# Kernel tuning notes

Hardware: AMD Instinct MI355X
Metric: run time of the kernel (lower is better)

The kernel has to match this reference:

```python
import jax, jax.numpy as jnp
import numpy as np

SEQ, BATCH, HID = 512, 64, 1024

def setup_inputs() -> dict:
    key = jax.random.key(0)
    ks = jax.random.split(key, 10)
    s2 = 1.0 / np.sqrt(2 * HID)
    s1 = 1.0 / np.sqrt(HID)
    return {
        "input": jax.random.normal(ks[0], (SEQ, BATCH, HID), dtype=jnp.float32),
        "prev_state": jax.random.normal(ks[1], (BATCH, HID), dtype=jnp.float32),
        # nn.Linear weights are [out, in], biases [out]
        "W_r": jax.random.uniform(ks[2], (HID, 2 * HID), jnp.float32, -s2, s2),
        "b_r": jax.random.uniform(ks[3], (HID,), jnp.float32, -s2, s2),
        "W_u": jax.random.uniform(ks[4], (HID, 2 * HID), jnp.float32, -s2, s2),
        "b_u": jax.random.uniform(ks[5], (HID,), jnp.float32, -s2, s2),
        "W_o": jax.random.uniform(ks[6], (HID, HID), jnp.float32, -s1, s1),
        "b_o": jax.random.uniform(ks[7], (HID,), jnp.float32, -s1, s1),
        "W_x": jax.random.uniform(ks[8], (HID, HID), jnp.float32, -s1, s1),
        "b_x": jax.random.uniform(ks[9], (HID,), jnp.float32, -s1, s1),
    }


def reference(input, prev_state, W_r, b_r, W_u, b_u, W_o, b_o, W_x, b_x):
    # input: [seq, batch, hid]; prev_state: [batch, hid]
    def step(h, x_t):
        xh = jnp.concatenate([x_t, h], axis=1)          # [batch, 2*hid]
        reset = jax.nn.sigmoid(xh @ W_r.T + b_r)
        update = jax.nn.sigmoid(xh @ W_u.T + b_u)
        cand = jnp.tanh((h @ W_o.T + b_o) * reset + (x_t @ W_x.T + b_x))
        new_h = (1.0 - update) * cand + update * h
        return new_h, new_h

    new_state, hidden_seq = jax.lax.scan(step, prev_state, input)
    return hidden_seq, new_state
```

## Files before the change

### kernel.cpp

```cpp
#include <hip/hip_runtime.h>
#include <hip/hip_bf16.h>

#define SEQ 512
#define BATCH 64
#define HID 1024

typedef __bf16 bf16x8 __attribute__((ext_vector_type(8)));
typedef __bf16 bf16x4 __attribute__((ext_vector_type(4)));
typedef float f32x4 __attribute__((ext_vector_type(4)));

__device__ __forceinline__ float sigm(float x) { return 1.0f / (1.0f + __expf(-x)); }
__device__ __forceinline__ float tanh_(float x) { return 2.0f / (1.0f + __expf(-2.0f * x)) - 1.0f; }

__device__ __forceinline__ void cload_b128(bf16x8* d, const __bf16* p) {
    asm volatile("global_load_dwordx4 %0, %1, off sc0 sc1" : "=v"(*d) : "v"(p));
}
__device__ __forceinline__ void cstore_b16(__bf16* p, __bf16 v) {
    unsigned short uv = __builtin_bit_cast(unsigned short, v);
    asm volatile("global_store_short %0, %1, off sc0 sc1" :: "v"(p), "v"(uv));
}
__device__ __forceinline__ void cstore_b32(unsigned* p, unsigned v) {
    asm volatile("global_store_dword %0, %1, off sc0 sc1" :: "v"(p), "v"(v));
}
__device__ __forceinline__ unsigned cload_b32(const unsigned* p) {
    unsigned r;
    asm volatile("global_load_dword %0, %1, off sc0 sc1\n\ts_waitcnt vmcnt(0)"
                 : "=v"(r) : "v"(p) : "memory");
    __builtin_amdgcn_sched_barrier(0);
    return r;
}
__device__ __forceinline__ void vmcnt0() {
    asm volatile("s_waitcnt vmcnt(0)" ::: "memory");
    __builtin_amdgcn_sched_barrier(0);
}

__global__ __launch_bounds__(256) void cvt_f32_bf16(const float* __restrict__ src,
                                                     __bf16* __restrict__ dst, int n)
{
    int i = (blockIdx.x * 256 + threadIdx.x) * 4;
    if (i < n) {
        f32x4 v = *(const f32x4*)(src + i);
        bf16x4 o;
        #pragma unroll
        for (int j = 0; j < 4; ++j) o[j] = (__bf16)v[j];
        *(bf16x4*)(dst + i) = o;
    }
}


__global__ __launch_bounds__(256) void gru_phaseA2(
    const __bf16* __restrict__ xb,
    const __bf16* __restrict__ Wrb, const __bf16* __restrict__ Wub,
    const __bf16* __restrict__ Wxb,
    const float* __restrict__ br, const float* __restrict__ bu,
    const float* __restrict__ bx, __bf16* __restrict__ G)
{
    __shared__ __bf16 Al[128 * 64];
    __shared__ __bf16 Bl[128 * 64];

    const int NT = 24;
    int mt = blockIdx.x / NT, nt = blockIdx.x % NT;
    int m0 = mt * 128, n0 = nt * 128;

    const __bf16* W; const float* bias; int wstride, nb, gate;
    if (n0 < HID)          { W = Wrb; bias = br; wstride = 2 * HID; nb = n0;           gate = 0; }
    else if (n0 < 2 * HID) { W = Wub; bias = bu; wstride = 2 * HID; nb = n0 - HID;     gate = 1; }
    else                   { W = Wxb; bias = bx; wstride = HID;     nb = n0 - 2 * HID; gate = 2; }

    const int tid = threadIdx.x;
    const int lane = tid & 63, w = tid >> 6;
    const int llo = lane & 15, lhi = lane >> 4;
    const int wm = (w & 1) * 64, wn = (w >> 1) * 64;

    f32x4 acc[4][4] = {};

    for (int k0 = 0; k0 < HID; k0 += 64) {
        __syncthreads();
        #pragma unroll
        for (int s = 0; s < 4; ++s) {
            int idx = s * 256 + tid;
            int r = idx >> 3, c16 = idx & 7;
            int eoff = (c16 * 8) ^ ((r & 7) << 3);
            const __bf16* ga = xb + (size_t)(m0 + r) * HID + k0 + eoff;
            char* la = (char*)Al + (size_t)(s * 256 + w * 64) * 16;
            __builtin_amdgcn_global_load_lds(
                (const __attribute__((address_space(1))) void*)ga,
                (__attribute__((address_space(3))) void*)la, 16, 0, 0);
        }
        #pragma unroll
        for (int s = 0; s < 4; ++s) {
            int idx = s * 256 + tid;
            int r = idx >> 3, c16 = idx & 7;
            int eoff = (c16 * 8) ^ ((r & 7) << 3);
            const __bf16* gb = W + (size_t)(nb + r) * wstride + k0 + eoff;
            char* lb = (char*)Bl + (size_t)(s * 256 + w * 64) * 16;
            __builtin_amdgcn_global_load_lds(
                (const __attribute__((address_space(1))) void*)gb,
                (__attribute__((address_space(3))) void*)lb, 16, 0, 0);
        }
        __syncthreads();

        #pragma unroll
        for (int kk = 0; kk < 2; ++kk) {
            bf16x8 a[4], b[4];
            #pragma unroll
            for (int mi = 0; mi < 4; ++mi) {
                int row = wm + mi * 16 + llo;
                a[mi] = *(const bf16x8*)((const char*)Al + row * 128
                          + ((kk * 64 + lhi * 16) ^ ((row & 7) << 4)));
            }
            #pragma unroll
            for (int ni = 0; ni < 4; ++ni) {
                int row = wn + ni * 16 + llo;
                b[ni] = *(const bf16x8*)((const char*)Bl + row * 128
                          + ((kk * 64 + lhi * 16) ^ ((row & 7) << 4)));
            }
            #pragma unroll
            for (int mi = 0; mi < 4; ++mi)
                #pragma unroll
                for (int ni = 0; ni < 4; ++ni)
                    acc[mi][ni] = __builtin_amdgcn_mfma_f32_16x16x32_bf16(a[mi], b[ni], acc[mi][ni], 0, 0, 0);
        }
    }

    #pragma unroll
    for (int ni = 0; ni < 4; ++ni) {
        int cg0 = nb + wn + ni * 16;
        int jn = cg0 >> 4;
        float bv = bias[cg0 + llo];
        #pragma unroll
        for (int mi = 0; mi < 4; ++mi) {
            #pragma unroll
            for (int i = 0; i < 4; ++i) {
                int m = m0 + wm + mi * 16 + lhi * 4 + i;
                int tt = m >> 6, b = m & 63;
                size_t addr = ((((size_t)tt * 8 + (b >> 3)) * 64 + jn) * 3 + gate) * 128
                            + (b & 7) * 16 + llo;
                G[addr] = (__bf16)(acc[mi][ni][i] + bv);
            }
        }
    }
}

__global__ __launch_bounds__(256) void gru_phaseA_f32(
    const float* __restrict__ xf,
    const __bf16* __restrict__ Wrb, const __bf16* __restrict__ Wub,
    const __bf16* __restrict__ Wxb,
    const float* __restrict__ br, const float* __restrict__ bu,
    const float* __restrict__ bx, __bf16* __restrict__ G)
{
    const int NT = (3 * HID) / 64;
    int mt = blockIdx.x / NT;
    int nt = blockIdx.x % NT;
    int m0 = mt * 128, n0 = nt * 64;

    const __bf16* W; const float* bias; int wstride, nb, gate;
    if (n0 < HID)          { W = Wrb; bias = br; wstride = 2 * HID; nb = n0;           gate = 0; }
    else if (n0 < 2 * HID) { W = Wub; bias = bu; wstride = 2 * HID; nb = n0 - HID;     gate = 1; }
    else                   { W = Wxb; bias = bx; wstride = HID;     nb = n0 - 2 * HID; gate = 2; }

    int lane = threadIdx.x & 63, w = threadIdx.x >> 6;
    int llo = lane & 15, lhi = lane >> 4;
    int wm = (w & 1) * 64, wn = (w >> 1) * 32;

    f32x4 acc[4][2] = {};
    #pragma unroll 2
    for (int k0 = 0; k0 < HID; k0 += 32) {
        int ka = k0 + lhi * 8;
        bf16x8 af[4], bfr[2];
        #pragma unroll
        for (int mi = 0; mi < 4; ++mi) {
            size_t roff = (size_t)(m0 + wm + mi * 16 + llo) * HID + ka;
            f32x4 lo = *(const f32x4*)(xf + roff);
            f32x4 hi = *(const f32x4*)(xf + roff + 4);
            #pragma unroll
            for (int jj = 0; jj < 4; ++jj) { af[mi][jj] = (__bf16)lo[jj]; af[mi][4 + jj] = (__bf16)hi[jj]; }
        }
        #pragma unroll
        for (int ni = 0; ni < 2; ++ni)
            bfr[ni] = *(const bf16x8*)(W + (size_t)(nb + wn + ni * 16 + llo) * wstride + ka);
        #pragma unroll
        for (int mi = 0; mi < 4; ++mi)
            #pragma unroll
            for (int ni = 0; ni < 2; ++ni)
                acc[mi][ni] = __builtin_amdgcn_mfma_f32_16x16x32_bf16(af[mi], bfr[ni], acc[mi][ni], 0, 0, 0);
    }
    #pragma unroll
    for (int ni = 0; ni < 2; ++ni) {
        int cg0 = nb + wn + ni * 16;
        int jn = cg0 >> 4;
        float bv = bias[cg0 + llo];
        #pragma unroll
        for (int mi = 0; mi < 4; ++mi) {
            #pragma unroll
            for (int i = 0; i < 4; ++i) {
                int m = m0 + wm + mi * 16 + lhi * 4 + i;
                int tt = m >> 6, b = m & 63;
                size_t addr = ((((size_t)tt * 8 + (b >> 3)) * 64 + jn) * 3 + gate) * 128
                            + (b & 7) * 16 + llo;
                G[addr] = (__bf16)(acc[mi][ni][i] + bv);
            }
        }
    }
}

__global__ __launch_bounds__(256) void gru_init(const float* __restrict__ prev,
                                                __bf16* __restrict__ hg,
                                                unsigned* __restrict__ flags)
{
    int i = blockIdx.x * 256 + threadIdx.x;
    if (i < 512 * 32) flags[i] = 0u;
    if (i < BATCH * HID) hg[i] = (__bf16)prev[i];
}

__global__ __launch_bounds__(256, 2) void gru_phaseB(
    const __bf16* __restrict__ Wrb, const __bf16* __restrict__ Wub,
    const __bf16* __restrict__ Wob, const float* __restrict__ bo,
    const float* __restrict__ prev, const __bf16* __restrict__ G,
    __bf16* __restrict__ hg, unsigned* __restrict__ flags,
    float* __restrict__ out)
{
    __shared__ float gbuf[2][3][4][128];
    __shared__ __bf16 Gld[2][384];

    const int gwg = blockIdx.x;
    const int j = gwg & 63, rg = gwg >> 6;
    const int tid = threadIdx.x;
    const int lane = tid & 63, ks = tid >> 6;
    const int llo = lane & 15, lhi = lane >> 4;

    bf16x8 wV[3][8];
    {
        const __bf16* w0 = Wrb + (size_t)(16 * j + llo) * (2 * HID) + HID + ks * 256 + lhi * 8;
        const __bf16* w1 = Wub + (size_t)(16 * j + llo) * (2 * HID) + HID + ks * 256 + lhi * 8;
        const __bf16* w2 = Wob + (size_t)(16 * j + llo) * HID + ks * 256 + lhi * 8;
        #pragma unroll
        for (int kk = 0; kk < 8; ++kk) {
            wV[0][kk] = *(const bf16x8*)(w0 + kk * 32);
            wV[1][kk] = *(const bf16x8*)(w1 + kk * 32);
            wV[2][kk] = *(const bf16x8*)(w2 + kk * 32);
        }
    }

    const int erow = 2 * ks + ((lane >> 4) & 1);
    const int ecol = lane & 15;
    float hf = 0.f, bov = 0.f;
    if (lane < 32) {
        hf = prev[(size_t)(8 * rg + erow) * HID + 16 * j + ecol];
        bov = bo[16 * j + ecol];
    }

    if (ks == 0 && lane < 48) {
        const __bf16* gsrc = G + (((size_t)0 * 8 + rg) * 64 + j) * 384 + lane * 8;
        __builtin_amdgcn_global_load_lds(
            (const __attribute__((address_space(1))) void*)gsrc,
            (__attribute__((address_space(3))) void*)((char*)&Gld[0][0] + lane * 16),
            16, 0, 0);
    }

    for (int t = 0; t < SEQ; ++t) {
        const int p = t & 1;
        if (t > 0) {
            const unsigned* fp = flags + (size_t)(rg * 64 + 16 * ks + llo) * 32;
            int guard = 0;
            for (;;) {
                unsigned v = cload_b32(fp);
                if (__all((int)(v >= (unsigned)t))) break;
                if (++guard >= (1 << 20)) break;
            }
        }
        const __bf16* hk = hg + (size_t)p * (BATCH * HID)
                         + (size_t)(8 * rg + (llo & 7)) * HID + ks * 256 + lhi * 8;
        bf16x8 hv[8];
        #pragma unroll
        for (int kk = 0; kk < 8; ++kk) cload_b128(&hv[kk], hk + kk * 32);
        vmcnt0();
        f32x4 aR = {}, aU = {}, aO = {};
        #pragma unroll
        for (int kk = 0; kk < 8; ++kk) {
            aR = __builtin_amdgcn_mfma_f32_16x16x32_bf16(hv[kk], wV[0][kk], aR, 0, 0, 0);
            aU = __builtin_amdgcn_mfma_f32_16x16x32_bf16(hv[kk], wV[1][kk], aU, 0, 0, 0);
            aO = __builtin_amdgcn_mfma_f32_16x16x32_bf16(hv[kk], wV[2][kk], aO, 0, 0, 0);
        }
        if (lhi < 2) {
            #pragma unroll
            for (int i = 0; i < 4; ++i) {
                gbuf[p][0][ks][(lhi * 4 + i) * 16 + llo] = aR[i];
                gbuf[p][1][ks][(lhi * 4 + i) * 16 + llo] = aU[i];
                gbuf[p][2][ks][(lhi * 4 + i) * 16 + llo] = aO[i];
            }
        }
        __syncthreads();

        float hnew = 0.f;
        if (lane < 32) {
            int idx = erow * 16 + ecol;
            float sR = gbuf[p][0][0][idx] + gbuf[p][0][1][idx] + gbuf[p][0][2][idx] + gbuf[p][0][3][idx];
            float sU = gbuf[p][1][0][idx] + gbuf[p][1][1][idx] + gbuf[p][1][2][idx] + gbuf[p][1][3][idx];
            float sO = gbuf[p][2][0][idx] + gbuf[p][2][1][idx] + gbuf[p][2][2][idx] + gbuf[p][2][3][idx];
            float gr = (float)Gld[p][0 * 128 + idx];
            float gu = (float)Gld[p][1 * 128 + idx];
            float gx = (float)Gld[p][2 * 128 + idx];
            float r = sigm(sR + gr);
            float u = sigm(sU + gu);
            float c = tanh_((sO + bov) * r + gx);
            hnew = (1.0f - u) * c + u * hf;
            hf = hnew;
            cstore_b16(hg + (size_t)(p ^ 1) * (BATCH * HID)
                          + (size_t)(8 * rg + erow) * HID + 16 * j + ecol, (__bf16)hnew);
        }
        __syncthreads();
        if (tid == 0)
            cstore_b32(flags + (size_t)(rg * 64 + j) * 32, (unsigned)(t + 1));
        if (ks == 0 && lane < 48 && t + 1 < SEQ) {
            const __bf16* gsrc = G + (((size_t)(t + 1) * 8 + rg) * 64 + j) * 384 + lane * 8;
            __builtin_amdgcn_global_load_lds(
                (const __attribute__((address_space(1))) void*)gsrc,
                (__attribute__((address_space(3))) void*)((char*)&Gld[p ^ 1][0] + lane * 16),
                16, 0, 0);
        }
        if (lane < 32) {
            __builtin_nontemporal_store(hnew,
                out + ((size_t)t * BATCH + 8 * rg + erow) * HID + 16 * j + ecol);
            if (t == SEQ - 1)
                __builtin_nontemporal_store(hnew,
                    out + ((size_t)SEQ * BATCH + 8 * rg + erow) * HID + 16 * j + ecol);
        }
    }
}

extern "C" void kernel_launch(void* const* d_in, const int* in_sizes, int n_in,
                              void* d_out, int out_size, void* d_ws, size_t ws_size,
                              hipStream_t stream) {
    (void)in_sizes; (void)n_in; (void)out_size;
    const float* x    = (const float*)d_in[0];
    const float* prev = (const float*)d_in[1];
    const float* Wr   = (const float*)d_in[2];
    const float* br   = (const float*)d_in[3];
    const float* Wu   = (const float*)d_in[4];
    const float* bu   = (const float*)d_in[5];
    const float* Wo   = (const float*)d_in[6];
    const float* bo   = (const float*)d_in[7];
    const float* Wx   = (const float*)d_in[8];
    const float* bx   = (const float*)d_in[9];
    float* out = (float*)d_out;

    const size_t G_ELEMS  = (size_t)SEQ * BATCH * 3 * HID;
    const size_t WR_ELEMS = (size_t)HID * 2 * HID;
    const size_t WO_ELEMS = (size_t)HID * HID;
    char* ws = (char*)d_ws;
    size_t off = 0;
    __bf16* G   = (__bf16*)(ws + off); off += G_ELEMS * 2;
    __bf16* Wrb = (__bf16*)(ws + off); off += WR_ELEMS * 2;
    __bf16* Wub = (__bf16*)(ws + off); off += WR_ELEMS * 2;
    __bf16* Wob = (__bf16*)(ws + off); off += WO_ELEMS * 2;
    __bf16* Wxb = (__bf16*)(ws + off); off += WO_ELEMS * 2;
    __bf16* hg  = (__bf16*)(ws + off); off += (size_t)2 * BATCH * HID * 2;
    unsigned* flags = (unsigned*)(ws + off); off += 512 * 32 * 4;
    const size_t X_ELEMS = (size_t)SEQ * BATCH * HID;
    bool use_xb = (ws_size >= off + X_ELEMS * 2);
    __bf16* xb = (__bf16*)(ws + off);

    cvt_f32_bf16<<<(int)(WR_ELEMS / 4 / 256), 256, 0, stream>>>(Wr, Wrb, (int)WR_ELEMS);
    cvt_f32_bf16<<<(int)(WR_ELEMS / 4 / 256), 256, 0, stream>>>(Wu, Wub, (int)WR_ELEMS);
    cvt_f32_bf16<<<(int)(WO_ELEMS / 4 / 256), 256, 0, stream>>>(Wo, Wob, (int)WO_ELEMS);
    cvt_f32_bf16<<<(int)(WO_ELEMS / 4 / 256), 256, 0, stream>>>(Wx, Wxb, (int)WO_ELEMS);
    if (use_xb)
        cvt_f32_bf16<<<(int)(X_ELEMS / 4 / 256), 256, 0, stream>>>(x, xb, (int)X_ELEMS);

    gru_init<<<(BATCH * HID) / 256, 256, 0, stream>>>(prev, hg, flags);

    if (use_xb) {
        gru_phaseA2<<<256 * 24, 256, 0, stream>>>(xb, Wrb, Wub, Wxb, br, bu, bx, G);
    } else {
        int gridA = (SEQ * BATCH / 128) * ((3 * HID) / 64);
        gru_phaseA_f32<<<gridA, 256, 0, stream>>>(x, Wrb, Wub, Wxb, br, bu, bx, G);
    }

    gru_phaseB<<<512, 256, 0, stream>>>(Wrb, Wub, Wob, bo, prev, G, hg, flags, out);
}
```

Before: 2.265 ms.

## Use per-wave packed step flags and batch output stores per eight steps

The cross-workgroup step flags are repacked into a dense 2048-entry layout, so a polling wave reads 64 adjacent flags (16 producers × 4 waves) instead of strided, padded slots. Each wave now publishes its own flag right after draining its hidden-state stores, which removes the second __syncthreads from the per-step critical path. Output writes to the hidden sequence are buffered in registers and issued every eight steps. The goal is to shorten the serial per-timestep latency, at the cost of correctness resting more on per-wave memory-ordering and more live registers.

```diff
diff --git a/kernel.cpp b/kernel.cpp
--- a/kernel.cpp
+++ b/kernel.cpp
@@ -209,7 +209,7 @@
                                                 unsigned* __restrict__ flags)
 {
     int i = blockIdx.x * 256 + threadIdx.x;
-    if (i < 512 * 32) flags[i] = 0u;
+    if (i < 2048) flags[i] = 0u;
     if (i < BATCH * HID) hg[i] = (__bf16)prev[i];
 }
 
@@ -250,6 +250,9 @@
         bov = bo[16 * j + ecol];
     }
 
+    unsigned* fstore = flags + (size_t)(rg * 4 + (j >> 4)) * 64 + (j & 15) * 4 + ks;
+    const unsigned* fpoll = flags + (size_t)(rg * 4 + ks) * 64 + (lane & 15) * 4 + (lane >> 4);
+
     if (ks == 0 && lane < 48) {
         const __bf16* gsrc = G + (((size_t)0 * 8 + rg) * 64 + j) * 384 + lane * 8;
         __builtin_amdgcn_global_load_lds(
@@ -258,72 +261,79 @@
             16, 0, 0);
     }
 
-    for (int t = 0; t < SEQ; ++t) {
-        const int p = t & 1;
-        if (t > 0) {
-            const unsigned* fp = flags + (size_t)(rg * 64 + 16 * ks + llo) * 32;
-            int guard = 0;
-            for (;;) {
-                unsigned v = cload_b32(fp);
-                if (__all((int)(v >= (unsigned)t))) break;
-                if (++guard >= (1 << 20)) break;
-            }
-        }
-        const __bf16* hk = hg + (size_t)p * (BATCH * HID)
-                         + (size_t)(8 * rg + (llo & 7)) * HID + ks * 256 + lhi * 8;
-        bf16x8 hv[8];
-        #pragma unroll
-        for (int kk = 0; kk < 8; ++kk) cload_b128(&hv[kk], hk + kk * 32);
-        vmcnt0();
-        f32x4 aR = {}, aU = {}, aO = {};
-        #pragma unroll
-        for (int kk = 0; kk < 8; ++kk) {
-            aR = __builtin_amdgcn_mfma_f32_16x16x32_bf16(hv[kk], wV[0][kk], aR, 0, 0, 0);
-            aU = __builtin_amdgcn_mfma_f32_16x16x32_bf16(hv[kk], wV[1][kk], aU, 0, 0, 0);
-            aO = __builtin_amdgcn_mfma_f32_16x16x32_bf16(hv[kk], wV[2][kk], aO, 0, 0, 0);
-        }
-        if (lhi < 2) {
-            #pragma unroll
-            for (int i = 0; i < 4; ++i) {
-                gbuf[p][0][ks][(lhi * 4 + i) * 16 + llo] = aR[i];
-                gbuf[p][1][ks][(lhi * 4 + i) * 16 + llo] = aU[i];
-                gbuf[p][2][ks][(lhi * 4 + i) * 16 + llo] = aO[i];
-            }
-        }
-        __syncthreads();
-
-        float hnew = 0.f;
+    float ob[8];
+    for (int t0 = 0; t0 < SEQ; t0 += 8) {
+        #pragma unroll
+        for (int s = 0; s < 8; ++s) {
+            const int t = t0 + s;
+            const int p = t & 1;
+            if (t > 0) {
+                int guard = 0;
+                for (;;) {
+                    unsigned v = cload_b32(fpoll);
+                    if (__all((int)(v >= (unsigned)t))) break;
+                    if (++guard >= (1 << 20)) break;
+                }
+            }
+            const __bf16* hk = hg + (size_t)p * (BATCH * HID)
+                             + (size_t)(8 * rg + (llo & 7)) * HID + ks * 256 + lhi * 8;
+            bf16x8 hv[8];
+            #pragma unroll
+            for (int kk = 0; kk < 8; ++kk) cload_b128(&hv[kk], hk + kk * 32);
+            vmcnt0();
+            f32x4 aR = {}, aU = {}, aO = {};
+            #pragma unroll
+            for (int kk = 0; kk < 8; ++kk) {
+                aR = __builtin_amdgcn_mfma_f32_16x16x32_bf16(hv[kk], wV[0][kk], aR, 0, 0, 0);
+                aU = __builtin_amdgcn_mfma_f32_16x16x32_bf16(hv[kk], wV[1][kk], aU, 0, 0, 0);
+                aO = __builtin_amdgcn_mfma_f32_16x16x32_bf16(hv[kk], wV[2][kk], aO, 0, 0, 0);
+            }
+            if (lhi < 2) {
+                #pragma unroll
+                for (int i = 0; i < 4; ++i) {
+                    gbuf[p][0][ks][(lhi * 4 + i) * 16 + llo] = aR[i];
+                    gbuf[p][1][ks][(lhi * 4 + i) * 16 + llo] = aU[i];
+                    gbuf[p][2][ks][(lhi * 4 + i) * 16 + llo] = aO[i];
+                }
+            }
+            __syncthreads();
+
+            float hnew = 0.f;
+            if (lane < 32) {
+                int idx = erow * 16 + ecol;
+                float sR = gbuf[p][0][0][idx] + gbuf[p][0][1][idx] + gbuf[p][0][2][idx] + gbuf[p][0][3][idx];
+                float sU = gbuf[p][1][0][idx] + gbuf[p][1][1][idx] + gbuf[p][1][2][idx] + gbuf[p][1][3][idx];
+                float sO = gbuf[p][2][0][idx] + gbuf[p][2][1][idx] + gbuf[p][2][2][idx] + gbuf[p][2][3][idx];
+                float gr = (float)Gld[p][0 * 128 + idx];
+                float gu = (float)Gld[p][1 * 128 + idx];
+                float gx = (float)Gld[p][2 * 128 + idx];
+                float r = sigm(sR + gr);
+                float u = sigm(sU + gu);
+                float c = tanh_((sO + bov) * r + gx);
+                hnew = (1.0f - u) * c + u * hf;
+                hf = hnew;
+                cstore_b16(hg + (size_t)(p ^ 1) * (BATCH * HID)
+                              + (size_t)(8 * rg + erow) * HID + 16 * j + ecol, (__bf16)hnew);
+            }
+            ob[s] = hnew;
+            vmcnt0();
+            if (lane == 0) cstore_b32(fstore, (unsigned)(t + 1));
+            if (ks == 0 && lane < 48 && t + 1 < SEQ) {
+                const __bf16* gsrc = G + (((size_t)(t + 1) * 8 + rg) * 64 + j) * 384 + lane * 8;
+                __builtin_amdgcn_global_load_lds(
+                    (const __attribute__((address_space(1))) void*)gsrc,
+                    (__attribute__((address_space(3))) void*)((char*)&Gld[p ^ 1][0] + lane * 16),
+                    16, 0, 0);
+            }
+        }
         if (lane < 32) {
-            int idx = erow * 16 + ecol;
-            float sR = gbuf[p][0][0][idx] + gbuf[p][0][1][idx] + gbuf[p][0][2][idx] + gbuf[p][0][3][idx];
-            float sU = gbuf[p][1][0][idx] + gbuf[p][1][1][idx] + gbuf[p][1][2][idx] + gbuf[p][1][3][idx];
-            float sO = gbuf[p][2][0][idx] + gbuf[p][2][1][idx] + gbuf[p][2][2][idx] + gbuf[p][2][3][idx];
-            float gr = (float)Gld[p][0 * 128 + idx];
-            float gu = (float)Gld[p][1 * 128 + idx];
-            float gx = (float)Gld[p][2 * 128 + idx];
-            float r = sigm(sR + gr);
-            float u = sigm(sU + gu);
-            float c = tanh_((sO + bov) * r + gx);
-            hnew = (1.0f - u) * c + u * hf;
-            hf = hnew;
-            cstore_b16(hg + (size_t)(p ^ 1) * (BATCH * HID)
-                          + (size_t)(8 * rg + erow) * HID + 16 * j + ecol, (__bf16)hnew);
-        }
-        __syncthreads();
-        if (tid == 0)
-            cstore_b32(flags + (size_t)(rg * 64 + j) * 32, (unsigned)(t + 1));
-        if (ks == 0 && lane < 48 && t + 1 < SEQ) {
-            const __bf16* gsrc = G + (((size_t)(t + 1) * 8 + rg) * 64 + j) * 384 + lane * 8;
-            __builtin_amdgcn_global_load_lds(
-                (const __attribute__((address_space(1))) void*)gsrc,
-                (__attribute__((address_space(3))) void*)((char*)&Gld[p ^ 1][0] + lane * 16),
-                16, 0, 0);
-        }
-        if (lane < 32) {
-            __builtin_nontemporal_store(hnew,
-                out + ((size_t)t * BATCH + 8 * rg + erow) * HID + 16 * j + ecol);
-            if (t == SEQ - 1)
-                __builtin_nontemporal_store(hnew,
+            #pragma unroll
+            for (int s = 0; s < 8; ++s) {
+                __builtin_nontemporal_store(ob[s],
+                    out + ((size_t)(t0 + s) * BATCH + 8 * rg + erow) * HID + 16 * j + ecol);
+            }
+            if (t0 + 8 == SEQ)
+                __builtin_nontemporal_store(ob[7],
                     out + ((size_t)SEQ * BATCH + 8 * rg + erow) * HID + 16 * j + ecol);
         }
     }
@@ -356,7 +366,7 @@
     __bf16* Wob = (__bf16*)(ws + off); off += WO_ELEMS * 2;
     __bf16* Wxb = (__bf16*)(ws + off); off += WO_ELEMS * 2;
     __bf16* hg  = (__bf16*)(ws + off); off += (size_t)2 * BATCH * HID * 2;
-    unsigned* flags = (unsigned*)(ws + off); off += 512 * 32 * 4;
+    unsigned* flags = (unsigned*)(ws + off); off += 2048 * 4;
     const size_t X_ELEMS = (size_t)SEQ * BATCH * HID;
     bool use_xb = (ws_size >= off + X_ELEMS * 2);
     __bf16* xb = (__bf16*)(ws + off);
```

New measurement: 3.511 ms. 1.55x slower.
